# Kernel optimization log

Hardware: AMD Instinct MI355X
Metric: run time of the kernel (lower is better)

## Reference

```python
import jax, jax.numpy as jnp
import numpy as np

B, S, D = 2, 2048, 2048
H, HK = 16, 4          # n_heads, n_kv_heads
DK = D // H            # 128
REP = H // HK


def setup_inputs() -> dict:
    key = jax.random.key(0)
    ks = jax.random.split(key, 9)
    x = jax.random.normal(ks[0], (B, S, D), dtype=jnp.float32)
    # RoPE tables: [max_seq_len, d_k/2]
    inv_freq = 1.0 / (10000.0 ** (jnp.arange(0, DK, 2, dtype=jnp.float32) / DK))
    t = jnp.arange(S, dtype=jnp.float32)
    freqs = jnp.outer(t, inv_freq)  # [S, DK/2]
    freqs_cos = jnp.cos(freqs)
    freqs_sin = jnp.sin(freqs)
    sc = 0.02
    return {
        "x": x,
        "freqs_cos": freqs_cos,
        "freqs_sin": freqs_sin,
        "wq_w": jax.random.normal(ks[1], (D, D), dtype=jnp.float32) * sc,
        "wq_b": jnp.zeros((D,), dtype=jnp.float32),
        "wk_w": jax.random.normal(ks[2], (HK * DK, D), dtype=jnp.float32) * sc,
        "wk_b": jnp.zeros((HK * DK,), dtype=jnp.float32),
        "wv_w": jax.random.normal(ks[3], (HK * DK, D), dtype=jnp.float32) * sc,
        "wv_b": jnp.zeros((HK * DK,), dtype=jnp.float32),
        "wo_w": jax.random.normal(ks[4], (D, D), dtype=jnp.float32) * sc,
        "wo_b": jnp.zeros((D,), dtype=jnp.float32),
    }


def _apply_rope(t, cos, sin):
    # t: [b, h, s, dk]; cos/sin: [1, 1, s, dk/2]; interleaved pairs (even=real, odd=imag)
    tr = t[..., 0::2]
    ti = t[..., 1::2]
    out_r = tr * cos - ti * sin
    out_i = tr * sin + ti * cos
    return jnp.stack([out_r, out_i], axis=-1).reshape(t.shape)


def reference(x, freqs_cos, freqs_sin, wq_w, wq_b, wk_w, wk_b, wv_w, wv_b, wo_w, wo_b):
    b, s, d = x.shape
    q = (x @ wq_w.T + wq_b).reshape(b, s, H, DK).transpose(0, 2, 1, 3)   # [b,H,s,dk]
    k = (x @ wk_w.T + wk_b).reshape(b, s, HK, DK).transpose(0, 2, 1, 3)  # [b,HK,s,dk]
    v = (x @ wv_w.T + wv_b).reshape(b, s, HK, DK).transpose(0, 2, 1, 3)

    cos = freqs_cos[:s][None, None]  # [1,1,s,dk/2]
    sin = freqs_sin[:s][None, None]
    q = _apply_rope(q, cos, sin)
    k = _apply_rope(k, cos, sin)

    # GQA: group q heads by kv head instead of materializing repeat_kv
    qg = q.reshape(b, HK, REP, s, DK)
    scores = jnp.einsum("bgrqd,bgkd->bgrqk", qg, k) / jnp.sqrt(jnp.float32(DK))
    causal = jnp.triu(jnp.full((s, s), -jnp.inf, dtype=scores.dtype), k=1)
    attn = jax.nn.softmax(scores + causal, axis=-1)  # dropout=0.0 -> no-op
    out = jnp.einsum("bgrqk,bgkd->bgrqd", attn, v)   # [b,HK,REP,s,dk]
    out = out.reshape(b, H, s, DK).transpose(0, 2, 1, 3).reshape(b, s, d)
    return out @ wo_w.T + wo_b
```

## Files before the change

### kernel.cpp

```cpp
#include <hip/hip_runtime.h>

#define BDIM 2
#define SDIM 2048
#define DDIM 2048
#define HQ 16
#define HKV 4
#define DKH 128
#define NKV 512
#define NQKV 3072
#define MROWS 4096

typedef __attribute__((ext_vector_type(8))) short bf16x8;
typedef __attribute__((ext_vector_type(4))) float f32x4;
typedef __attribute__((ext_vector_type(8))) unsigned short u16x8;
typedef __attribute__((ext_vector_type(4))) unsigned short u16x4;

#define AS1 __attribute__((address_space(1)))
#define AS3 __attribute__((address_space(3)))

__device__ __forceinline__ unsigned short f2bf(float f) {
    union { float f; unsigned int u; } v; v.f = f;
    unsigned int r = v.u + 0x7FFFu + ((v.u >> 16) & 1u);
    return (unsigned short)(r >> 16);
}
__device__ __forceinline__ float bf2f(unsigned short u) {
    union { unsigned int u; float f; } v; v.u = ((unsigned int)u) << 16;
    return v.f;
}
__device__ __forceinline__ unsigned int pack2bf(float a, float b) {
    return (unsigned int)f2bf(a) | ((unsigned int)f2bf(b) << 16);
}

#define NX   ((size_t)MROWS * DDIM)
#define NWQ  ((size_t)DDIM * DDIM)
#define NWKV ((size_t)NKV * DDIM)
#define CAST_BLOCKS 18432
__global__ void cast_all(const float* __restrict__ x, const float* __restrict__ wq,
                         const float* __restrict__ wk, const float* __restrict__ wv,
                         const float* __restrict__ wo, unsigned short* __restrict__ dst,
                         const float* __restrict__ qb, const float* __restrict__ kb,
                         const float* __restrict__ vb, float* __restrict__ b3) {
    if (blockIdx.x >= CAST_BLOCKS) {
        int i = (blockIdx.x - CAST_BLOCKS) * 256 + threadIdx.x;
        if (i < DDIM) b3[i] = qb[i];
        else if (i < DDIM + NKV) b3[i] = kb[i - DDIM];
        else if (i < NQKV) b3[i] = vb[i - DDIM - NKV];
        return;
    }
    size_t i = ((size_t)blockIdx.x * blockDim.x + threadIdx.x) * 4;
    const size_t N0 = NX, N1 = N0 + NWQ, N2 = N1 + NWKV, N3 = N2 + NWKV;
    const float* src; size_t off;
    if (i < N0)      { src = x;  off = i; }
    else if (i < N1) { src = wq; off = i - N0; }
    else if (i < N2) { src = wk; off = i - N1; }
    else if (i < N3) { src = wv; off = i - N2; }
    else             { src = wo; off = i - N3; }
    float4 v = *(const float4*)(src + off);
    u16x4 o;
    o[0] = f2bf(v.x); o[1] = f2bf(v.y); o[2] = f2bf(v.z); o[3] = f2bf(v.w);
    *(u16x4*)(dst + i) = o;
}

__global__ void rope_trans(unsigned short* __restrict__ buf,
                           const float* __restrict__ cosT, const float* __restrict__ sinT,
                           unsigned short* __restrict__ Vt, float qscale) {
    if (blockIdx.x < MROWS) {
        int r = blockIdx.x, pos = r & (SDIM - 1);
        int col0 = threadIdx.x * 8;
        unsigned short* p = buf + (size_t)r * NQKV + col0;
        int i0 = (col0 & 127) >> 1;
        float4 c4 = *(const float4*)(cosT + pos * 64 + i0);
        float4 s4 = *(const float4*)(sinT + pos * 64 + i0);
        float sc = (col0 < DDIM) ? qscale : 1.f;
        u16x8 v = *(const u16x8*)p;
        u16x8 o;
        float cc[4] = {c4.x, c4.y, c4.z, c4.w}, ss[4] = {s4.x, s4.y, s4.z, s4.w};
#pragma unroll
        for (int k = 0; k < 4; ++k) {
            float xr = bf2f(v[2 * k]), xi = bf2f(v[2 * k + 1]);
            o[2 * k]     = f2bf((xr * cc[k] - xi * ss[k]) * sc);
            o[2 * k + 1] = f2bf((xr * ss[k] + xi * cc[k]) * sc);
        }
        *(u16x8*)p = o;
    } else {
        __shared__ unsigned short T[32][33];
        if (threadIdx.x >= 256) return;
        int t = blockIdx.x - MROWS;
        int s0 = (t & 63) * 32, d0 = ((t >> 6) & 15) * 32, b = t >> 10;
        int c = threadIdx.x & 31, r4 = threadIdx.x >> 5;
        for (int rr = r4; rr < 32; rr += 8)
            T[rr][c] = buf[(size_t)(b * SDIM + s0 + rr) * NQKV + (DDIM + NKV) + d0 + c];
        __syncthreads();
        int cp = ((c & 0x0C) << 1) | ((c & 0x10) >> 2) | (c & 3);
        for (int rr = r4; rr < 32; rr += 8)
            Vt[(size_t)(b * NKV + d0 + rr) * SDIM + s0 + cp] = T[c][rr];
    }
}

template <int BF16OUT, int BM, int BN, int WM, int WN>
__global__ __launch_bounds__(512, 2) void gemm_rp(
    const unsigned short* __restrict__ A,
    const unsigned short* __restrict__ Bm,
    const float* __restrict__ bias,
    void* __restrict__ Cv,
    int pitch, int Kdim) {
    constexpr int MF = BM / WM / 16;
    constexpr int NF = BN / WN / 16;
    constexpr int AI = BM / 128;
    constexpr int BI = BN / 128;
    constexpr int L  = AI + BI;
    constexpr int BUFS = (BM + BN) * 32;

    __shared__ unsigned short Ls[3 * BUFS];

    const int tid = threadIdx.x;
    const int lane = tid & 63;
    const int wid = tid >> 6;
    const int ml = lane & 15, quad = lane >> 4;
    const int wm = wid / WN, wn = wid % WN;

    const int gx = gridDim.x;
    const int nwg = gx * gridDim.y;
    int w0 = blockIdx.y * gx + blockIdx.x;
    int wsw = (nwg & 7) ? w0 : ((w0 & 7) * (nwg >> 3) + (w0 >> 3));
    const int m0 = (wsw / gx) * BM, n0 = (wsw % gx) * BN;

    const int NT = Kdim >> 5;

    const int sr = tid >> 2;
    const int sk = ((tid & 3) ^ ((tid >> 3) & 3)) * 8;
    const unsigned short* Ag0 = A + (size_t)(m0 + sr) * Kdim + sk;
    const unsigned short* Bg0 = Bm + (size_t)(n0 + sr) * Kdim + sk;

    const int xsl = (quad ^ ((ml >> 1) & 3)) * 8;
    const int afr0 = wm * (BM / WM) + ml;
    const int bfr0 = BM * 32 + (wn * (BN / WN) + ml) * 32;

    f32x4 acc[MF][NF] = {};
    bf16x8 afA[MF], bfA[NF], afB[MF], bfB[NF];

#define STAGE(ib, kt2)                                                                          \
    do {                                                                                        \
        unsigned short* lb = &Ls[(ib) * BUFS];                                                  \
        _Pragma("unroll")                                                                       \
        for (int ll = 0; ll < AI; ++ll)                                                         \
            __builtin_amdgcn_global_load_lds(                                                   \
                (const AS1 unsigned int*)(Ag0 + (size_t)(ll * 128) * Kdim + (kt2)),             \
                (AS3 unsigned int*)(lb + ll * 4096 + tid * 8), 16, 0, 0);                       \
        _Pragma("unroll")                                                                       \
        for (int ll = 0; ll < BI; ++ll)                                                         \
            __builtin_amdgcn_global_load_lds(                                                   \
                (const AS1 unsigned int*)(Bg0 + (size_t)(ll * 128) * Kdim + (kt2)),             \
                (AS3 unsigned int*)(lb + BM * 32 + ll * 4096 + tid * 8), 16, 0, 0);             \
    } while (0)
#define READF(afX, bfX, ib)                                                                     \
    do {                                                                                        \
        const unsigned short* lb = &Ls[(ib) * BUFS];                                            \
        _Pragma("unroll")                                                                       \
        for (int mf = 0; mf < MF; ++mf)                                                         \
            afX[mf] = *(const bf16x8*)(lb + (afr0 + mf * 16) * 32 + xsl);                       \
        _Pragma("unroll")                                                                       \
        for (int nf = 0; nf < NF; ++nf)                                                         \
            bfX[nf] = *(const bf16x8*)(lb + bfr0 + nf * 16 * 32 + xsl);                         \
    } while (0)
#define MMALL(afX, bfX)                                                                         \
    do {                                                                                        \
        _Pragma("unroll")                                                                       \
        for (int mf = 0; mf < MF; ++mf)                                                         \
            _Pragma("unroll")                                                                   \
            for (int nf = 0; nf < NF; ++nf)                                                     \
                acc[mf][nf] = __builtin_amdgcn_mfma_f32_16x16x32_bf16(                          \
                    afX[mf], bfX[nf], acc[mf][nf], 0, 0, 0);                                    \
    } while (0)
#define WAIT_VM_L()                                                                             \
    do {                                                                                        \
        if constexpr (L == 3) asm volatile("s_waitcnt vmcnt(3)" ::: "memory");                  \
        else                  asm volatile("s_waitcnt vmcnt(4)" ::: "memory");                  \
    } while (0)
#define BODY(CAF, CBF, NAF, NBF, G)                                                             \
    do {                                                                                        \
        const int Gs = (G) + 2, Gr = (G) + 1;                                                   \
        if (Gs < NT) { STAGE(Gs % 3, Gs * 32); WAIT_VM_L(); }                                   \
        else         { asm volatile("s_waitcnt vmcnt(0)" ::: "memory"); }                       \
        __builtin_amdgcn_sched_barrier(0);                                                      \
        __builtin_amdgcn_s_barrier();                                                           \
        READF(NAF, NBF, Gr % 3);                                                                \
        __builtin_amdgcn_s_setprio(1);                                                          \
        MMALL(CAF, CBF);                                                                        \
        __builtin_amdgcn_s_setprio(0);                                                          \
        asm volatile("s_waitcnt lgkmcnt(0)" ::: "memory");                                      \
        __builtin_amdgcn_sched_barrier(0);                                                      \
    } while (0)

    STAGE(0, 0);
    STAGE(1, 32);
    WAIT_VM_L();
    __builtin_amdgcn_s_barrier();
    READF(afA, bfA, 0);
    asm volatile("s_waitcnt lgkmcnt(0)" ::: "memory");
    __builtin_amdgcn_sched_barrier(0);

    for (int G = 0; G < NT; G += 2) {
        BODY(afA, bfA, afB, bfB, G);
        BODY(afB, bfB, afA, bfA, G + 1);
    }
#undef STAGE
#undef READF
#undef MMALL
#undef WAIT_VM_L
#undef BODY

#pragma unroll
    for (int nf = 0; nf < NF; ++nf) {
        const int col = n0 + wn * (BN / WN) + nf * 16 + ml;
        const float bj = bias[col];
#pragma unroll
        for (int mf = 0; mf < MF; ++mf) {
            const int row0 = m0 + wm * (BM / WM) + mf * 16 + quad * 4;
#pragma unroll
            for (int rr = 0; rr < 4; ++rr) {
                float v = acc[mf][nf][rr] + bj;
                if (BF16OUT)
                    ((unsigned short*)Cv)[(size_t)(row0 + rr) * pitch + col] = f2bf(v);
                else
                    ((float*)Cv)[(size_t)(row0 + rr) * pitch + col] = v;
            }
        }
    }
}

__global__ __launch_bounds__(256, 2) void attn_fwd(
    const unsigned short* __restrict__ Qp,
    const unsigned short* __restrict__ Kp,
    const unsigned short* __restrict__ Vt,
    unsigned short* __restrict__ O) {
    const int l = blockIdx.x;
    const int j = l & 15;
    const int h = (l >> 4) & 15;
    const int b = l >> 8;
    const int g = h >> 2;
    const int jh = 31 - j;
    const int tid = threadIdx.x;
    const int w = tid >> 6, lane = tid & 63;
    const int ml = lane & 15, quad = lane >> 4;
    const int rsub = lane >> 2, seg = lane & 3;
    const int pr = w >> 1;
    const int wsub = w & 1;
    const int ssw = (rsub >> 1) & 3;
    const int xsw = (ml >> 1) & 3;

    __shared__ unsigned short Ks[2][4 * 64 * 32];
    __shared__ unsigned short Vs[2][2 * 128 * 32];

    int myqt = pr ? j : jh;
    int q0 = myqt * 64 + wsub * 32;

    bf16x8 aq[2][4];
    auto load_q = [&](int qt) {
#pragma unroll
        for (int g2 = 0; g2 < 2; ++g2) {
            const size_t qrow = (size_t)(b * SDIM + qt * 64 + wsub * 32 + g2 * 16 + ml);
#pragma unroll
            for (int kc = 0; kc < 4; ++kc)
                aq[g2][kc] = *(const bf16x8*)(Qp + qrow * NQKV + h * DKH + kc * 32 + quad * 8);
        }
    };
    load_q(myqt);

    f32x4 o_acc[2][8] = {};
    float l_acc[2] = {0.f, 0.f};

    auto store_out = [&](int qt) {
#pragma unroll
        for (int g2 = 0; g2 < 2; ++g2) {
            float lt = l_acc[g2];
            lt += __shfl_xor(lt, 16);
            lt += __shfl_xor(lt, 32);
            float inv = 1.f / lt;
            size_t rowbase = (size_t)(b * SDIM + qt * 64 + wsub * 32 + g2 * 16 + ml) * DDIM + h * DKH + quad * 4;
#pragma unroll
            for (int dt = 0; dt < 8; ++dt) {
                u16x4 ov;
#pragma unroll
                for (int r = 0; r < 4; ++r)
                    ov[r] = f2bf(o_acc[g2][dt][r] * inv);
                *(u16x4*)(O + rowbase + dt * 16) = ov;
            }
        }
    };

    for (int it = 0; it < 17; ++it) {
        int kt;
        if (pr == 0)       kt = it;
        else if (it <= j)  kt = it;
        else if (it <= 15) kt = 16 + it - j;
        else               kt = -1;

        __syncthreads();
        if (kt >= 0) {
            const int kb = kt * 64;
#pragma unroll
            for (int kc = 0; kc < 4; ++kc)
#pragma unroll
                for (int rh = 0; rh < 2; ++rh)
                    __builtin_amdgcn_global_load_lds(
                        (const AS1 unsigned int*)(Kp + (size_t)(b * SDIM + kb + rh * 32 + wsub * 16 + rsub) * NQKV + g * DKH + kc * 32 + (seg ^ ssw) * 8),
                        (AS3 unsigned int*)(&Ks[pr][kc * 2048 + rh * 1024 + wsub * 512 + lane * 8]), 16, 0, 0);
#pragma unroll
            for (int c = 0; c < 8; ++c) {
                int u = wsub * 8 + c, kc2 = u >> 3, rg = u & 7;
                __builtin_amdgcn_global_load_lds(
                    (const AS1 unsigned int*)(Vt + (size_t)(b * NKV + g * DKH + rg * 16 + rsub) * SDIM + kb + kc2 * 32 + (seg ^ ssw) * 8),
                    (AS3 unsigned int*)(&Vs[pr][u * 512 + lane * 8]), 16, 0, 0);
            }
        }
        __syncthreads();

        if (pr == 1 && it == j + 1) {
            store_out(j);
            myqt = jh; q0 = myqt * 64 + wsub * 32;
            load_q(jh);
#pragma unroll
            for (int g2 = 0; g2 < 2; ++g2) {
                l_acc[g2] = 0.f;
#pragma unroll
                for (int dt = 0; dt < 8; ++dt) o_acc[g2][dt] = (f32x4){0.f, 0.f, 0.f, 0.f};
            }
        }

        if (kt >= 0) {
            const int kb = kt * 64;
            __builtin_amdgcn_s_setprio(1);
            f32x4 st[2][4];
#pragma unroll
            for (int t = 0; t < 4; ++t) {
                bf16x8 ak[4];
#pragma unroll
                for (int kc = 0; kc < 4; ++kc)
                    ak[kc] = *(const bf16x8*)&Ks[pr][kc * 2048 + (t * 16 + ml) * 32 + (quad ^ xsw) * 8];
#pragma unroll
                for (int g2 = 0; g2 < 2; ++g2) {
                    f32x4 sc = {};
#pragma unroll
                    for (int kc = 0; kc < 4; ++kc)
                        sc = __builtin_amdgcn_mfma_f32_16x16x32_bf16(ak[kc], aq[g2][kc], sc, 0, 0, 0);
                    st[g2][t] = sc;
                }
            }

            if (kb + 63 > q0) {
#pragma unroll
                for (int g2 = 0; g2 < 2; ++g2) {
                    int qg = q0 + g2 * 16 + ml;
#pragma unroll
                    for (int t = 0; t < 4; ++t) {
                        int kvb = kb + t * 16 + quad * 4;
#pragma unroll
                        for (int r = 0; r < 4; ++r)
                            if (kvb + r > qg) st[g2][t][r] = -INFINITY;
                    }
                }
            }

            unsigned int pk[2][4][2];
#pragma unroll
            for (int g2 = 0; g2 < 2; ++g2) {
#pragma unroll
                for (int t = 0; t < 4; ++t) {
                    float p0 = __expf(st[g2][t][0] - 20.f);
                    float p1 = __expf(st[g2][t][1] - 20.f);
                    float p2 = __expf(st[g2][t][2] - 20.f);
                    float p3 = __expf(st[g2][t][3] - 20.f);
                    l_acc[g2] += (p0 + p1) + (p2 + p3);
                    pk[g2][t][0] = pack2bf(p0, p1);
                    pk[g2][t][1] = pack2bf(p2, p3);
                }
            }

#pragma unroll
            for (int c = 0; c < 2; ++c) {
                union { unsigned int u[4]; bf16x8 v; } pb[2];
#pragma unroll
                for (int g2 = 0; g2 < 2; ++g2) {
                    pb[g2].u[0] = pk[g2][2 * c][0];     pb[g2].u[1] = pk[g2][2 * c][1];
                    pb[g2].u[2] = pk[g2][2 * c + 1][0]; pb[g2].u[3] = pk[g2][2 * c + 1][1];
                }
#pragma unroll
                for (int dt = 0; dt < 8; ++dt) {
                    bf16x8 av = *(const bf16x8*)&Vs[pr][c * 4096 + (dt * 16 + ml) * 32 + (quad ^ xsw) * 8];
                    o_acc[0][dt] = __builtin_amdgcn_mfma_f32_16x16x32_bf16(av, pb[0].v, o_acc[0][dt], 0, 0, 0);
                    o_acc[1][dt] = __builtin_amdgcn_mfma_f32_16x16x32_bf16(av, pb[1].v, o_acc[1][dt], 0, 0, 0);
                }
            }
            __builtin_amdgcn_s_setprio(0);
        }
    }

    __syncthreads();
    float* Fo = (float*)&Ks[0][0];
    float* Fl = (float*)&Vs[0][0];
    if (pr == 0) {
#pragma unroll
        for (int g2 = 0; g2 < 2; ++g2) {
            Fl[(g2 * 2 + wsub) * 64 + lane] = l_acc[g2];
#pragma unroll
            for (int dt = 0; dt < 8; ++dt)
                *(f32x4*)&Fo[(g2 * 8 + dt) * 512 + wsub * 256 + lane * 4] = o_acc[g2][dt];
        }
    }
    __syncthreads();
    if (pr == 1) {
#pragma unroll
        for (int g2 = 0; g2 < 2; ++g2) {
            l_acc[g2] += Fl[(g2 * 2 + wsub) * 64 + lane];
#pragma unroll
            for (int dt = 0; dt < 8; ++dt) {
                f32x4 pa = *(const f32x4*)&Fo[(g2 * 8 + dt) * 512 + wsub * 256 + lane * 4];
#pragma unroll
                for (int r = 0; r < 4; ++r) o_acc[g2][dt][r] += pa[r];
            }
        }
        store_out(jh);
    }
}

extern "C" void kernel_launch(void* const* d_in, const int* in_sizes, int n_in,
                              void* d_out, int out_size, void* d_ws, size_t ws_size,
                              hipStream_t stream) {
    const float* x    = (const float*)d_in[0];
    const float* fcos = (const float*)d_in[1];
    const float* fsin = (const float*)d_in[2];
    const float* wq_w = (const float*)d_in[3];
    const float* wq_b = (const float*)d_in[4];
    const float* wk_w = (const float*)d_in[5];
    const float* wk_b = (const float*)d_in[6];
    const float* wv_w = (const float*)d_in[7];
    const float* wv_b = (const float*)d_in[8];
    const float* wo_w = (const float*)d_in[9];
    const float* wo_b = (const float*)d_in[10];
    float* out = (float*)d_out;

    char* ws = (char*)d_ws;
    size_t off = 0;
    auto alloc = [&](size_t bytes) {
        char* p = ws + off;
        off += (bytes + 255) & ~(size_t)255;
        return p;
    };
    unsigned short* xb  = (unsigned short*)alloc(NX * 2);
    unsigned short* W3  = (unsigned short*)alloc((size_t)NQKV * DDIM * 2);
    unsigned short* wob = (unsigned short*)alloc(NWQ * 2);
    float* b3           = (float*)alloc((size_t)NQKV * 4);
    unsigned short* qkv = (unsigned short*)alloc((size_t)MROWS * NQKV * 2);
    unsigned short* Vt  = (unsigned short*)alloc((size_t)BDIM * NKV * SDIM * 2);
    unsigned short* att = (unsigned short*)alloc((size_t)MROWS * DDIM * 2);

    cast_all<<<dim3(CAST_BLOCKS + 12), dim3(256), 0, stream>>>(
        x, wq_w, wk_w, wv_w, wo_w, xb, wq_b, wk_b, wv_b, b3);

    gemm_rp<1, 128, 384, 1, 8><<<dim3(NQKV / 384, MROWS / 128), 512, 0, stream>>>(
        xb, W3, b3, qkv, NQKV, DDIM);

    const float scale = 0.08838834764831845f;
    rope_trans<<<dim3(MROWS + 2048), dim3(320), 0, stream>>>(qkv, fcos, fsin, Vt, scale);

    attn_fwd<<<dim3(512), dim3(256), 0, stream>>>(qkv, qkv + DDIM, Vt, att);

    gemm_rp<0, 256, 128, 4, 2><<<dim3(DDIM / 128, MROWS / 256), 512, 0, stream>>>(
        att, wob, wo_b, out, DDIM, DDIM);
}
```

Measured before the change: 295.8 us.

## Fuse RoPE into QKV GEMM epilogue and use new double-buffered output GEMM

RoPE rotation and Q scaling move into the QKV GEMM epilogue, using a lane shuffle to fetch each value's interleaved partner. This removes the separate read-modify-write pass over Q and K, leaving only a standalone V transpose kernel. The output projection switches to a new GEMM kernel with split-half LDS double buffering, global-to-LDS direct loads and a 2x4 wave layout. The epilogue now does scattered cos/sin loads per element, and the new GEMM's pipeline may behave differently from the old triple-buffered one.

```diff
diff --git a/kernel.cpp b/kernel.cpp
--- a/kernel.cpp
+++ b/kernel.cpp
@@ -61,49 +61,28 @@
     *(u16x4*)(dst + i) = o;
 }
 
-__global__ void rope_trans(unsigned short* __restrict__ buf,
-                           const float* __restrict__ cosT, const float* __restrict__ sinT,
-                           unsigned short* __restrict__ Vt, float qscale) {
-    if (blockIdx.x < MROWS) {
-        int r = blockIdx.x, pos = r & (SDIM - 1);
-        int col0 = threadIdx.x * 8;
-        unsigned short* p = buf + (size_t)r * NQKV + col0;
-        int i0 = (col0 & 127) >> 1;
-        float4 c4 = *(const float4*)(cosT + pos * 64 + i0);
-        float4 s4 = *(const float4*)(sinT + pos * 64 + i0);
-        float sc = (col0 < DDIM) ? qscale : 1.f;
-        u16x8 v = *(const u16x8*)p;
-        u16x8 o;
-        float cc[4] = {c4.x, c4.y, c4.z, c4.w}, ss[4] = {s4.x, s4.y, s4.z, s4.w};
-#pragma unroll
-        for (int k = 0; k < 4; ++k) {
-            float xr = bf2f(v[2 * k]), xi = bf2f(v[2 * k + 1]);
-            o[2 * k]     = f2bf((xr * cc[k] - xi * ss[k]) * sc);
-            o[2 * k + 1] = f2bf((xr * ss[k] + xi * cc[k]) * sc);
-        }
-        *(u16x8*)p = o;
-    } else {
-        __shared__ unsigned short T[32][33];
-        if (threadIdx.x >= 256) return;
-        int t = blockIdx.x - MROWS;
-        int s0 = (t & 63) * 32, d0 = ((t >> 6) & 15) * 32, b = t >> 10;
-        int c = threadIdx.x & 31, r4 = threadIdx.x >> 5;
-        for (int rr = r4; rr < 32; rr += 8)
-            T[rr][c] = buf[(size_t)(b * SDIM + s0 + rr) * NQKV + (DDIM + NKV) + d0 + c];
-        __syncthreads();
-        int cp = ((c & 0x0C) << 1) | ((c & 0x10) >> 2) | (c & 3);
-        for (int rr = r4; rr < 32; rr += 8)
-            Vt[(size_t)(b * NKV + d0 + rr) * SDIM + s0 + cp] = T[c][rr];
-    }
-}
-
-template <int BF16OUT, int BM, int BN, int WM, int WN>
+__global__ void v_trans(const unsigned short* __restrict__ buf,
+                        unsigned short* __restrict__ Vt) {
+    __shared__ unsigned short T[32][33];
+    int t = blockIdx.x;
+    int s0 = (t & 63) * 32, d0 = ((t >> 6) & 15) * 32, b = t >> 10;
+    int c = threadIdx.x & 31, r4 = threadIdx.x >> 5;
+    for (int rr = r4; rr < 32; rr += 8)
+        T[rr][c] = buf[(size_t)(b * SDIM + s0 + rr) * NQKV + (DDIM + NKV) + d0 + c];
+    __syncthreads();
+    int cp = ((c & 0x0C) << 1) | ((c & 0x10) >> 2) | (c & 3);
+    for (int rr = r4; rr < 32; rr += 8)
+        Vt[(size_t)(b * NKV + d0 + rr) * SDIM + s0 + cp] = T[c][rr];
+}
+
+template <int BF16OUT, int BM, int BN, int WM, int WN, int ROPE>
 __global__ __launch_bounds__(512, 2) void gemm_rp(
     const unsigned short* __restrict__ A,
     const unsigned short* __restrict__ Bm,
     const float* __restrict__ bias,
     void* __restrict__ Cv,
-    int pitch, int Kdim) {
+    int pitch, int Kdim,
+    const float* __restrict__ cosT, const float* __restrict__ sinT, float qscale) {
     constexpr int MF = BM / WM / 16;
     constexpr int NF = BN / WN / 16;
     constexpr int AI = BM / 128;
@@ -214,12 +193,170 @@
     for (int nf = 0; nf < NF; ++nf) {
         const int col = n0 + wn * (BN / WN) + nf * 16 + ml;
         const float bj = bias[col];
+        const bool doRope = ROPE && (col < DDIM + NKV);
+        const float sc = (ROPE && col < DDIM) ? qscale : 1.f;
+        const int i0 = (col & 127) >> 1;
 #pragma unroll
         for (int mf = 0; mf < MF; ++mf) {
             const int row0 = m0 + wm * (BM / WM) + mf * 16 + quad * 4;
 #pragma unroll
             for (int rr = 0; rr < 4; ++rr) {
                 float v = acc[mf][nf][rr] + bj;
+                if constexpr (ROPE) {
+                    float vp = __shfl_xor(v, 1);
+                    if (doRope) {
+                        const int pos = (row0 + rr) & (SDIM - 1);
+                        const float c = cosT[pos * 64 + i0];
+                        const float s = sinT[pos * 64 + i0];
+                        v = (col & 1) ? (vp * s + v * c) : (v * c - vp * s);
+                    }
+                    v *= sc;
+                }
+                if (BF16OUT)
+                    ((unsigned short*)Cv)[(size_t)(row0 + rr) * pitch + col] = f2bf(v);
+                else
+                    ((float*)Cv)[(size_t)(row0 + rr) * pitch + col] = v;
+            }
+        }
+    }
+}
+
+template <int BF16OUT, int BM, int BN, int WM, int WN>
+__global__ __launch_bounds__(512, 2) void gemm2b(
+    const unsigned short* __restrict__ A,
+    const unsigned short* __restrict__ Bm,
+    const float* __restrict__ bias,
+    void* __restrict__ Cv,
+    int pitch, int Kdim) {
+    constexpr int MF = BM / WM / 16;
+    constexpr int NFRAG = BN / WN / 16;
+    constexpr int AH = BM / 128;
+    constexpr int BH = BN / 128;
+    constexpr int AHR = BM / 2;
+    constexpr int BHR = BN / 2;
+
+    __shared__ unsigned short As[2][2][AHR * 64];
+    __shared__ unsigned short Bs[2][2][BHR * 64];
+
+    const int tid = threadIdx.x;
+    const int lane = tid & 63;
+    const int wid = tid >> 6;
+    const int ml = lane & 15, quad = lane >> 4;
+    const int wm = wid / WN, wn = wid % WN;
+    const int bhf = wn / (WN / 2);
+    const int brb = (wn % (WN / 2)) * (BN / WN);
+
+    const int gx = gridDim.x;
+    const int nwg = gx * gridDim.y;
+    int w0 = blockIdx.y * gx + blockIdx.x;
+    int wsw = (nwg & 7) ? w0 : ((w0 & 7) * (nwg >> 3) + (w0 >> 3));
+    const int m0 = (wsw / gx) * BM, n0 = (wsw % gx) * BN;
+
+    const int NT = Kdim >> 6;
+    const int xr = ml & 7;
+
+    const int sr = tid >> 3;
+    const int sk = ((tid & 7) ^ (sr & 7)) * 8;
+    const unsigned short* Ag0 = A + (size_t)(m0 + sr) * Kdim + sk;
+    const unsigned short* Bg0 = Bm + (size_t)(n0 + sr) * Kdim + sk;
+
+    f32x4 acc[MF][NFRAG] = {};
+
+#define STG_A(bf, hf, kt)                                                                       \
+    do {                                                                                        \
+        _Pragma("unroll")                                                                       \
+        for (int ll = 0; ll < AH; ++ll)                                                         \
+            __builtin_amdgcn_global_load_lds(                                                   \
+                (const AS1 unsigned int*)(Ag0 + (size_t)((hf) * AHR + ll * 64) * Kdim + (kt)),  \
+                (AS3 unsigned int*)(&As[bf][hf][ll * 4096 + tid * 8]), 16, 0, 0);               \
+    } while (0)
+#define STG_B(bf, hf, kt)                                                                       \
+    do {                                                                                        \
+        _Pragma("unroll")                                                                       \
+        for (int ll = 0; ll < BH; ++ll)                                                         \
+            __builtin_amdgcn_global_load_lds(                                                   \
+                (const AS1 unsigned int*)(Bg0 + (size_t)((hf) * BHR + ll * 64) * Kdim + (kt)),  \
+                (AS3 unsigned int*)(&Bs[bf][hf][ll * 4096 + tid * 8]), 16, 0, 0);               \
+    } while (0)
+#define WAIT_VM_STEADY()                                                                        \
+    do {                                                                                        \
+        if constexpr (BH == 1)      asm volatile("s_waitcnt vmcnt(2)" ::: "memory");            \
+        else if constexpr (BH == 2) asm volatile("s_waitcnt vmcnt(4)" ::: "memory");            \
+        else                        asm volatile("s_waitcnt vmcnt(6)" ::: "memory");            \
+    } while (0)
+
+    STG_B(0, 0, 0); STG_B(0, 1, 0);
+    STG_A(0, 0, 0); STG_A(0, 1, 0);
+    if (NT > 1) {
+        STG_B(1, 0, 64); STG_B(1, 1, 64);
+        WAIT_VM_STEADY();
+    } else {
+        asm volatile("s_waitcnt vmcnt(0)" ::: "memory");
+    }
+    __builtin_amdgcn_s_barrier();
+    __builtin_amdgcn_sched_barrier(0);
+
+    for (int G = 0; G < NT; ++G) {
+        const int cur = G & 1, nxt = cur ^ 1;
+        const int ktA = (G + 1) * 64, ktB = (G + 2) * 64;
+        const unsigned short* Bh = Bs[cur][bhf];
+
+        bf16x8 bfr[NFRAG][2];
+#pragma unroll
+        for (int nj = 0; nj < NFRAG; ++nj)
+#pragma unroll
+            for (int kk = 0; kk < 2; ++kk)
+                bfr[nj][kk] = *(const bf16x8*)&Bh[(brb + nj * 16 + ml) * 64 + ((kk * 4 + quad) ^ xr) * 8];
+
+        bf16x8 af[MF][2];
+#pragma unroll
+        for (int mf = 0; mf < MF; ++mf) {
+            const int arow0 = wm * (BM / WM) + mf * 16;
+            const int ahf = arow0 / AHR;
+            const int arin = arow0 % AHR + ml;
+#pragma unroll
+            for (int kk = 0; kk < 2; ++kk)
+                af[mf][kk] = *(const bf16x8*)&As[cur][ahf][arin * 64 + ((kk * 4 + quad) ^ xr) * 8];
+        }
+
+        if (G + 1 < NT) { STG_A(nxt, 0, ktA); STG_A(nxt, 1, ktA); }
+
+        __builtin_amdgcn_s_setprio(1);
+#pragma unroll
+        for (int kk = 0; kk < 2; ++kk)
+#pragma unroll
+            for (int mf = 0; mf < MF; ++mf)
+#pragma unroll
+                for (int nj = 0; nj < NFRAG; ++nj)
+                    acc[mf][nj] = __builtin_amdgcn_mfma_f32_16x16x32_bf16(
+                        af[mf][kk], bfr[nj][kk], acc[mf][nj], 0, 0, 0);
+        __builtin_amdgcn_s_setprio(0);
+
+        asm volatile("s_waitcnt lgkmcnt(0)" ::: "memory");
+        __builtin_amdgcn_sched_barrier(0);
+        __builtin_amdgcn_s_barrier();
+
+        if (G + 2 < NT) { STG_B(cur, 0, ktB); STG_B(cur, 1, ktB); }
+        if (G < NT - 2)       { WAIT_VM_STEADY(); }
+        else if (G == NT - 2) { asm volatile("s_waitcnt vmcnt(0)" ::: "memory"); }
+        __builtin_amdgcn_sched_barrier(0);
+        __builtin_amdgcn_s_barrier();
+        __builtin_amdgcn_sched_barrier(0);
+    }
+#undef STG_A
+#undef STG_B
+#undef WAIT_VM_STEADY
+
+#pragma unroll
+    for (int nj = 0; nj < NFRAG; ++nj) {
+        const int col = n0 + wn * (BN / WN) + nj * 16 + ml;
+        const float bj = bias[col];
+#pragma unroll
+        for (int mf = 0; mf < MF; ++mf) {
+            const int row0 = m0 + wm * (BM / WM) + mf * 16 + quad * 4;
+#pragma unroll
+            for (int rr = 0; rr < 4; ++rr) {
+                float v = acc[mf][nj][rr] + bj;
                 if (BF16OUT)
                     ((unsigned short*)Cv)[(size_t)(row0 + rr) * pitch + col] = f2bf(v);
                 else
@@ -458,14 +595,15 @@
     cast_all<<<dim3(CAST_BLOCKS + 12), dim3(256), 0, stream>>>(
         x, wq_w, wk_w, wv_w, wo_w, xb, wq_b, wk_b, wv_b, b3);
 
-    gemm_rp<1, 128, 384, 1, 8><<<dim3(NQKV / 384, MROWS / 128), 512, 0, stream>>>(
-        xb, W3, b3, qkv, NQKV, DDIM);
-
     const float scale = 0.08838834764831845f;
-    rope_trans<<<dim3(MROWS + 2048), dim3(320), 0, stream>>>(qkv, fcos, fsin, Vt, scale);
+
+    gemm_rp<1, 128, 384, 1, 8, 1><<<dim3(NQKV / 384, MROWS / 128), 512, 0, stream>>>(
+        xb, W3, b3, qkv, NQKV, DDIM, fcos, fsin, scale);
+
+    v_trans<<<dim3(2048), dim3(256), 0, stream>>>(qkv, Vt);
 
     attn_fwd<<<dim3(512), dim3(256), 0, stream>>>(qkv, qkv + DDIM, Vt, att);
 
-    gemm_rp<0, 256, 128, 4, 2><<<dim3(DDIM / 128, MROWS / 256), 512, 0, stream>>>(
+    gemm2b<0, 256, 128, 2, 4><<<dim3(DDIM / 128, MROWS / 256), 512, 0, stream>>>(
         att, wob, wo_b, out, DDIM, DDIM);
 }
```

After: 309.1 us. +4.5%, slower.
